# Optimization experiments

Measured on AMD Instinct MI355X. Metric: run time of the kernel, lower is better.

Reference implementation:

```python
import jax, jax.numpy as jnp
import numpy as np

B, F, T, L = 65536, 512, 8, 4


def setup_inputs() -> dict:
    key = jax.random.key(0)
    k1, k2, k3, k4, k5 = jax.random.split(key, 5)
    scale = 1.0 / np.sqrt(F)  # keep the 4-deep cross stack numerically tame
    return {
        "x": jax.random.normal(k1, (B, F), dtype=jnp.float32),
        "cross_w": jax.random.normal(k2, (L, F), dtype=jnp.float32) * scale,
        "cross_b": jax.random.normal(k3, (L, F), dtype=jnp.float32) * 0.1,
        "W_out": jax.random.normal(k4, (F, T), dtype=jnp.float32) * scale,
        "b_out": jax.random.normal(k5, (T,), dtype=jnp.float32) * 0.1,
    }


def reference(x, cross_w, cross_b, W_out, b_out):
    # DCN cross layers. torch does bmm(x0[:, :, None], x[:, None, :]) -> [B,F,F]
    # then tensordot with weights over the last axis; algebraically identical to
    # x0 * (x . w), which we compute directly (no O(B*F*F) intermediate).
    x0 = x
    for i in range(L):  # small fixed layer loop
        s = jnp.einsum("bf,f->b", x, cross_w[i])  # [B]
        x = x0 * s[:, None] + cross_b[i] + x
    return x @ W_out + b_out  # final Linear [B, T]
```

## Files before the change

kernel.cpp:

```cpp
#include <hip/hip_runtime.h>
#include <hip/hip_bf16.h>


typedef float v4f __attribute__((ext_vector_type(4)));
typedef float f32x4 __attribute__((ext_vector_type(4)));
typedef short s16x8 __attribute__((ext_vector_type(8)));

__device__ __forceinline__ short f2bf(float v) {
  return __builtin_bit_cast(short, __float2bfloat16(v));
}
__device__ __forceinline__ float bf2f(short s) {
  return __uint_as_float(((unsigned)(unsigned short)s) << 16);
}

template<int CTRL>
__device__ __forceinline__ float dpp_add(float v) {
  int t = __builtin_amdgcn_update_dpp(0, __float_as_int(v), CTRL, 0xF, 0xF, true);
  return v + __int_as_float(t);
}
__device__ __forceinline__ float wave_reduce(float v) {
  v = dpp_add<0x111>(v); v = dpp_add<0x112>(v); v = dpp_add<0x114>(v);
  v = dpp_add<0x118>(v); v = dpp_add<0x142>(v); v = dpp_add<0x143>(v);
  return v;
}

__global__ __launch_bounds__(256, 4) void cross_mfma(
    const float* __restrict__ x, const float* __restrict__ cw,
    const float* __restrict__ cb, const float* __restrict__ Wo,
    const float* __restrict__ bo, float* __restrict__ out)
{
  __shared__ s16x8 Bh[16][64];
  __shared__ s16x8 Bl[16][64];
  __shared__ float ct[4][16][17];
  __shared__ float egs[12];

  const int tid = threadIdx.x, lane = tid & 63, wv = tid >> 6;

  for (int slot = tid; slot < 1024; slot += 256) {
    const int s = slot >> 6, l = slot & 63;
    const int c = l & 15, k0 = s * 32 + ((l >> 4) << 3);
    float f[8];
    if (c < 4) {
      v4f a = *(const v4f*)(cw + c * 512 + k0);
      v4f b = *(const v4f*)(cw + c * 512 + k0 + 4);
      #pragma unroll
      for (int j = 0; j < 4; ++j) { f[j] = a[j]; f[4 + j] = b[j]; }
    } else if (c < 12) {
      #pragma unroll
      for (int j = 0; j < 8; ++j) f[j] = Wo[(k0 + j) * 8 + (c - 4)];
    } else {
      #pragma unroll
      for (int j = 0; j < 8; ++j) f[j] = 0.f;
    }
    s16x8 h, lo;
    #pragma unroll
    for (int j = 0; j < 8; ++j) {
      h[j]  = f2bf(f[j]);
      lo[j] = f2bf(f[j] - bf2f(h[j]));
    }
    Bh[s][l] = h;
    Bl[s][l] = lo;
  }

  if (wv == 0) {
    const int f0 = lane << 3;
    v4f d0a = *(const v4f*)(cb + f0),        d0b = *(const v4f*)(cb + f0 + 4);
    v4f c1a = *(const v4f*)(cb + 512 + f0),  c1b = *(const v4f*)(cb + 512 + f0 + 4);
    v4f c2a = *(const v4f*)(cb + 1024 + f0), c2b = *(const v4f*)(cb + 1024 + f0 + 4);
    v4f c3a = *(const v4f*)(cb + 1536 + f0), c3b = *(const v4f*)(cb + 1536 + f0 + 4);
    v4f w1a = *(const v4f*)(cw + 512 + f0),  w1b = *(const v4f*)(cw + 512 + f0 + 4);
    v4f w2a = *(const v4f*)(cw + 1024 + f0), w2b = *(const v4f*)(cw + 1024 + f0 + 4);
    v4f w3a = *(const v4f*)(cw + 1536 + f0), w3b = *(const v4f*)(cw + 1536 + f0 + 4);
    float e1p = 0.f, e2p = 0.f, e3p = 0.f;
    v4f dA = d0a, dB = d0b;
    #pragma unroll
    for (int e = 0; e < 4; ++e) e1p += dA[e] * w1a[e] + dB[e] * w1b[e];
    dA += c1a; dB += c1b;
    #pragma unroll
    for (int e = 0; e < 4; ++e) e2p += dA[e] * w2a[e] + dB[e] * w2b[e];
    dA += c2a; dB += c2b;
    #pragma unroll
    for (int e = 0; e < 4; ++e) e3p += dA[e] * w3a[e] + dB[e] * w3b[e];
    dA += c3a; dB += c3b;
    float gp[8] = {0.f,0.f,0.f,0.f,0.f,0.f,0.f,0.f};
    #pragma unroll
    for (int e = 0; e < 4; ++e) {
      const float* wra = Wo + (f0 + e) * 8;
      const float* wrb = Wo + (f0 + 4 + e) * 8;
      #pragma unroll
      for (int t = 0; t < 8; ++t) gp[t] += dA[e] * wra[t] + dB[e] * wrb[t];
    }
    e1p = wave_reduce(e1p); e2p = wave_reduce(e2p); e3p = wave_reduce(e3p);
    #pragma unroll
    for (int t = 0; t < 8; ++t) gp[t] = wave_reduce(gp[t]);
    if (lane == 63) {
      egs[0] = e1p; egs[1] = e2p; egs[2] = e3p;
      #pragma unroll
      for (int t = 0; t < 8; ++t) egs[3 + t] = gp[t] + bo[t];
    }
  }
  __syncthreads();

  const int row0 = (blockIdx.x << 6) + (wv << 4);
  const float* xr = x + (size_t)(row0 + (lane & 15)) * 512 + ((lane >> 4) << 3);
  const float e1 = egs[0], e2 = egs[1], e3 = egs[2];
  float gg[8];
  #pragma unroll
  for (int t = 0; t < 8; ++t) gg[t] = egs[3 + t];

  f32x4 acc = {0.f, 0.f, 0.f, 0.f};
  v4f pa = *(const v4f*)(xr), pb = *(const v4f*)(xr + 4);
  #pragma unroll
  for (int s = 0; s < 16; ++s) {
    v4f na = pa, nb = pb;
    if (s < 15) {
      na = *(const v4f*)(xr + (s + 1) * 32);
      nb = *(const v4f*)(xr + (s + 1) * 32 + 4);
    }
    const s16x8 bh = Bh[s][lane];
    const s16x8 bl = Bl[s][lane];
    s16x8 ah, al;
    #pragma unroll
    for (int j = 0; j < 4; ++j) {
      ah[j]     = f2bf(pa[j]); al[j]     = f2bf(pa[j] - bf2f(ah[j]));
      ah[4 + j] = f2bf(pb[j]); al[4 + j] = f2bf(pb[j] - bf2f(ah[4 + j]));
    }
    acc = __builtin_amdgcn_mfma_f32_16x16x32_bf16(ah, bh, acc, 0, 0, 0);
    acc = __builtin_amdgcn_mfma_f32_16x16x32_bf16(al, bh, acc, 0, 0, 0);
    acc = __builtin_amdgcn_mfma_f32_16x16x32_bf16(ah, bl, acc, 0, 0, 0);
    pa = na; pb = nb;
  }

  #pragma unroll
  for (int j = 0; j < 4; ++j)
    ct[wv][((lane >> 4) << 2) + j][lane & 15] = acc[j];
  if (lane < 16) {
    const float u0 = ct[wv][lane][0], u1 = ct[wv][lane][1];
    const float u2 = ct[wv][lane][2], u3 = ct[wv][lane][3];
    const float cc1 = 1.f + u0;
    const float cc2 = fmaf(cc1, u1, cc1) + e1;
    const float cc3 = fmaf(cc2, u2, cc2) + e2;
    const float cc4 = fmaf(cc3, u3, cc3) + e3;
    v4f o0, o1;
    #pragma unroll
    for (int t = 0; t < 4; ++t) {
      o0[t] = fmaf(cc4, ct[wv][lane][4 + t], gg[t]);
      o1[t] = fmaf(cc4, ct[wv][lane][8 + t], gg[4 + t]);
    }
    float* op = out + (size_t)(row0 + lane) * 8;
    *(v4f*)(op)     = o0;
    *(v4f*)(op + 4) = o1;
  }
}

extern "C" void kernel_launch(void* const* d_in, const int* in_sizes, int n_in,
                              void* d_out, int out_size, void* d_ws, size_t ws_size,
                              hipStream_t stream) {
  const float* x  = (const float*)d_in[0];
  const float* cw = (const float*)d_in[1];
  const float* cb = (const float*)d_in[2];
  const float* Wo = (const float*)d_in[3];
  const float* bo = (const float*)d_in[4];
  float* out = (float*)d_out;
  const int B = in_sizes[0] / 512;
  hipLaunchKernelGGL(cross_mfma, dim3(B >> 6), dim3(256), 0, stream,
                     x, cw, cb, Wo, bo, out);
}
```

Before: 30.63 us.

## Split weight-table prep into separate kernel and stream x with deeper prefetch

Moves the bf16 weight-table and bias-constant construction out of every block into a small pre-kernel that writes them to workspace. The main kernel then loads the table into registers, drops shared-memory staging and the block barrier, and prefetches x three steps ahead. It also removes the low-part correction on the weights, using two MFMAs per step instead of three. That lowers weight precision to bf16 plus a split of x only, and adds a second launch plus higher register pressure from 16 held fragments.

```diff
diff --git a/kernel.cpp b/kernel.cpp
--- a/kernel.cpp
+++ b/kernel.cpp
@@ -24,46 +24,35 @@
   return v;
 }
 
-__global__ __launch_bounds__(256, 4) void cross_mfma(
-    const float* __restrict__ x, const float* __restrict__ cw,
-    const float* __restrict__ cb, const float* __restrict__ Wo,
-    const float* __restrict__ bo, float* __restrict__ out)
+__global__ __launch_bounds__(64) void build_tab(
+    const float* __restrict__ cw, const float* __restrict__ cb,
+    const float* __restrict__ Wo, const float* __restrict__ bo, void* ws)
 {
-  __shared__ s16x8 Bh[16][64];
-  __shared__ s16x8 Bl[16][64];
-  __shared__ float ct[4][16][17];
-  __shared__ float egs[12];
+  s16x8* Bt = (s16x8*)ws;
+  float* egs = (float*)((char*)ws + 16384);
+  const int s = blockIdx.x, l = threadIdx.x;
+  const int c = l & 15, k0 = s * 32 + ((l >> 4) << 3);
 
-  const int tid = threadIdx.x, lane = tid & 63, wv = tid >> 6;
+  float f[8];
+  if (c < 4) {
+    v4f a = *(const v4f*)(cw + c * 512 + k0);
+    v4f b = *(const v4f*)(cw + c * 512 + k0 + 4);
+    #pragma unroll
+    for (int j = 0; j < 4; ++j) { f[j] = a[j]; f[4 + j] = b[j]; }
+  } else if (c < 12) {
+    #pragma unroll
+    for (int j = 0; j < 8; ++j) f[j] = Wo[(k0 + j) * 8 + (c - 4)];
+  } else {
+    #pragma unroll
+    for (int j = 0; j < 8; ++j) f[j] = 0.f;
+  }
+  s16x8 h;
+  #pragma unroll
+  for (int j = 0; j < 8; ++j) h[j] = f2bf(f[j]);
+  Bt[s * 64 + l] = h;
 
-  for (int slot = tid; slot < 1024; slot += 256) {
-    const int s = slot >> 6, l = slot & 63;
-    const int c = l & 15, k0 = s * 32 + ((l >> 4) << 3);
-    float f[8];
-    if (c < 4) {
-      v4f a = *(const v4f*)(cw + c * 512 + k0);
-      v4f b = *(const v4f*)(cw + c * 512 + k0 + 4);
-      #pragma unroll
-      for (int j = 0; j < 4; ++j) { f[j] = a[j]; f[4 + j] = b[j]; }
-    } else if (c < 12) {
-      #pragma unroll
-      for (int j = 0; j < 8; ++j) f[j] = Wo[(k0 + j) * 8 + (c - 4)];
-    } else {
-      #pragma unroll
-      for (int j = 0; j < 8; ++j) f[j] = 0.f;
-    }
-    s16x8 h, lo;
-    #pragma unroll
-    for (int j = 0; j < 8; ++j) {
-      h[j]  = f2bf(f[j]);
-      lo[j] = f2bf(f[j] - bf2f(h[j]));
-    }
-    Bh[s][l] = h;
-    Bl[s][l] = lo;
-  }
-
-  if (wv == 0) {
-    const int f0 = lane << 3;
+  if (s == 0) {
+    const int f0 = l << 3;
     v4f d0a = *(const v4f*)(cb + f0),        d0b = *(const v4f*)(cb + f0 + 4);
     v4f c1a = *(const v4f*)(cb + 512 + f0),  c1b = *(const v4f*)(cb + 512 + f0 + 4);
     v4f c2a = *(const v4f*)(cb + 1024 + f0), c2b = *(const v4f*)(cb + 1024 + f0 + 4);
@@ -93,47 +82,65 @@
     e1p = wave_reduce(e1p); e2p = wave_reduce(e2p); e3p = wave_reduce(e3p);
     #pragma unroll
     for (int t = 0; t < 8; ++t) gp[t] = wave_reduce(gp[t]);
-    if (lane == 63) {
+    if (l == 63) {
       egs[0] = e1p; egs[1] = e2p; egs[2] = e3p;
       #pragma unroll
       for (int t = 0; t < 8; ++t) egs[3 + t] = gp[t] + bo[t];
     }
   }
-  __syncthreads();
+}
 
-  const int row0 = (blockIdx.x << 6) + (wv << 4);
-  const float* xr = x + (size_t)(row0 + (lane & 15)) * 512 + ((lane >> 4) << 3);
+__global__ __launch_bounds__(256, 4) void cross_stream(
+    const float* __restrict__ x, const void* __restrict__ ws,
+    float* __restrict__ out)
+{
+  __shared__ float ct[4][16][17];
+
+  const int tid = threadIdx.x, lane = tid & 63, wv = tid >> 6;
+  const s16x8* Bt = (const s16x8*)ws;
+  const float* egs = (const float*)((const char*)ws + 16384);
+
+  s16x8 Bf[16];
+  #pragma unroll
+  for (int s = 0; s < 16; ++s) Bf[s] = Bt[s * 64 + lane];
+
   const float e1 = egs[0], e2 = egs[1], e3 = egs[2];
   float gg[8];
   #pragma unroll
   for (int t = 0; t < 8; ++t) gg[t] = egs[3 + t];
 
+  const int row0 = (blockIdx.x << 6) + (wv << 4);
+  const float* xr = x + (size_t)(row0 + (lane & 15)) * 512 + ((lane >> 4) << 3);
+
   f32x4 acc = {0.f, 0.f, 0.f, 0.f};
-  v4f pa = *(const v4f*)(xr), pb = *(const v4f*)(xr + 4);
+  v4f xa[3], xb[3];
+  #pragma unroll
+  for (int p = 0; p < 3; ++p) {
+    xa[p] = *(const v4f*)(xr + p * 32);
+    xb[p] = *(const v4f*)(xr + p * 32 + 4);
+  }
   #pragma unroll
   for (int s = 0; s < 16; ++s) {
-    v4f na = pa, nb = pb;
-    if (s < 15) {
-      na = *(const v4f*)(xr + (s + 1) * 32);
-      nb = *(const v4f*)(xr + (s + 1) * 32 + 4);
+    const int cur = s % 3;
+    const v4f pa = xa[cur], pb = xb[cur];
+    if (s + 3 < 16) {
+      xa[cur] = *(const v4f*)(xr + (s + 3) * 32);
+      xb[cur] = *(const v4f*)(xr + (s + 3) * 32 + 4);
     }
-    const s16x8 bh = Bh[s][lane];
-    const s16x8 bl = Bl[s][lane];
     s16x8 ah, al;
     #pragma unroll
     for (int j = 0; j < 4; ++j) {
       ah[j]     = f2bf(pa[j]); al[j]     = f2bf(pa[j] - bf2f(ah[j]));
       ah[4 + j] = f2bf(pb[j]); al[4 + j] = f2bf(pb[j] - bf2f(ah[4 + j]));
     }
-    acc = __builtin_amdgcn_mfma_f32_16x16x32_bf16(ah, bh, acc, 0, 0, 0);
-    acc = __builtin_amdgcn_mfma_f32_16x16x32_bf16(al, bh, acc, 0, 0, 0);
-    acc = __builtin_amdgcn_mfma_f32_16x16x32_bf16(ah, bl, acc, 0, 0, 0);
-    pa = na; pb = nb;
+    acc = __builtin_amdgcn_mfma_f32_16x16x32_bf16(ah, Bf[s], acc, 0, 0, 0);
+    acc = __builtin_amdgcn_mfma_f32_16x16x32_bf16(al, Bf[s], acc, 0, 0, 0);
   }
 
   #pragma unroll
   for (int j = 0; j < 4; ++j)
     ct[wv][((lane >> 4) << 2) + j][lane & 15] = acc[j];
+  __builtin_amdgcn_s_waitcnt(0);
   if (lane < 16) {
     const float u0 = ct[wv][lane][0], u1 = ct[wv][lane][1];
     const float u2 = ct[wv][lane][2], u3 = ct[wv][lane][3];
@@ -163,6 +170,8 @@
   const float* bo = (const float*)d_in[4];
   float* out = (float*)d_out;
   const int B = in_sizes[0] / 512;
-  hipLaunchKernelGGL(cross_mfma, dim3(B >> 6), dim3(256), 0, stream,
-                     x, cw, cb, Wo, bo, out);
+  hipLaunchKernelGGL(build_tab, dim3(16), dim3(64), 0, stream,
+                     cw, cb, Wo, bo, d_ws);
+  hipLaunchKernelGGL(cross_stream, dim3(B >> 6), dim3(256), 0, stream,
+                     x, d_ws, out);
 }
```

Result: slower. 31.37 us (+2.4%).

## Deepen x prefetch, drop low-bf16 weight split, compute constants per wave

Applied to the files above, without the earlier changes.

The x row chunks are now prefetched six steps ahead, with the first six loads issued before the shared-memory weight staging, so global latency overlaps setup. The low-order bf16 part of the weights is removed, which cuts one MFMA per step and halves the weight staging in LDS, at some cost in precision. Each wave now computes the bias-chain constants itself and broadcasts them with a shuffle, which removes the shared egs buffer and its dependence on wave 0. This adds redundant work across waves and raises register pressure from the 12 prefetch vectors.

```diff
diff --git a/kernel.cpp b/kernel.cpp
--- a/kernel.cpp
+++ b/kernel.cpp
@@ -24,20 +24,29 @@
   return v;
 }
 
-__global__ __launch_bounds__(256, 4) void cross_mfma(
+__global__ __launch_bounds__(256, 4) void cross_one(
     const float* __restrict__ x, const float* __restrict__ cw,
     const float* __restrict__ cb, const float* __restrict__ Wo,
     const float* __restrict__ bo, float* __restrict__ out)
 {
   __shared__ s16x8 Bh[16][64];
-  __shared__ s16x8 Bl[16][64];
   __shared__ float ct[4][16][17];
-  __shared__ float egs[12];
 
   const int tid = threadIdx.x, lane = tid & 63, wv = tid >> 6;
+  const int row0 = (blockIdx.x << 6) + (wv << 4);
+  const float* xr = x + (size_t)(row0 + (lane & 15)) * 512 + ((lane >> 4) << 3);
 
-  for (int slot = tid; slot < 1024; slot += 256) {
-    const int s = slot >> 6, l = slot & 63;
+  v4f xa[6], xb[6];
+  #pragma unroll
+  for (int p = 0; p < 6; ++p) {
+    xa[p] = *(const v4f*)(xr + p * 32);
+    xb[p] = *(const v4f*)(xr + p * 32 + 4);
+  }
+
+  #pragma unroll
+  for (int slot = 0; slot < 4; ++slot) {
+    const int s = (tid >> 6) + (slot << 2);
+    const int l = tid & 63;
     const int c = l & 15, k0 = s * 32 + ((l >> 4) << 3);
     float f[8];
     if (c < 4) {
@@ -52,17 +61,35 @@
       #pragma unroll
       for (int j = 0; j < 8; ++j) f[j] = 0.f;
     }
-    s16x8 h, lo;
+    s16x8 h;
     #pragma unroll
-    for (int j = 0; j < 8; ++j) {
-      h[j]  = f2bf(f[j]);
-      lo[j] = f2bf(f[j] - bf2f(h[j]));
+    for (int j = 0; j < 8; ++j) h[j] = f2bf(f[j]);
+    Bh[s][l] = h;
+  }
+  __syncthreads();
+
+  f32x4 acc = {0.f, 0.f, 0.f, 0.f};
+  #pragma unroll
+  for (int s = 0; s < 16; ++s) {
+    const int cur = s % 6;
+    const v4f pa = xa[cur], pb = xb[cur];
+    if (s + 6 < 16) {
+      xa[cur] = *(const v4f*)(xr + (s + 6) * 32);
+      xb[cur] = *(const v4f*)(xr + (s + 6) * 32 + 4);
     }
-    Bh[s][l] = h;
-    Bl[s][l] = lo;
+    const s16x8 bh = Bh[s][lane];
+    s16x8 ah, al;
+    #pragma unroll
+    for (int j = 0; j < 4; ++j) {
+      ah[j]     = f2bf(pa[j]); al[j]     = f2bf(pa[j] - bf2f(ah[j]));
+      ah[4 + j] = f2bf(pb[j]); al[4 + j] = f2bf(pb[j] - bf2f(ah[4 + j]));
+    }
+    acc = __builtin_amdgcn_mfma_f32_16x16x32_bf16(ah, bh, acc, 0, 0, 0);
+    acc = __builtin_amdgcn_mfma_f32_16x16x32_bf16(al, bh, acc, 0, 0, 0);
   }
 
-  if (wv == 0) {
+  float e1, e2, e3, gg[8];
+  {
     const int f0 = lane << 3;
     v4f d0a = *(const v4f*)(cb + f0),        d0b = *(const v4f*)(cb + f0 + 4);
     v4f c1a = *(const v4f*)(cb + 512 + f0),  c1b = *(const v4f*)(cb + 512 + f0 + 4);
@@ -93,47 +120,15 @@
     e1p = wave_reduce(e1p); e2p = wave_reduce(e2p); e3p = wave_reduce(e3p);
     #pragma unroll
     for (int t = 0; t < 8; ++t) gp[t] = wave_reduce(gp[t]);
-    if (lane == 63) {
-      egs[0] = e1p; egs[1] = e2p; egs[2] = e3p;
-      #pragma unroll
-      for (int t = 0; t < 8; ++t) egs[3 + t] = gp[t] + bo[t];
-    }
-  }
-  __syncthreads();
-
-  const int row0 = (blockIdx.x << 6) + (wv << 4);
-  const float* xr = x + (size_t)(row0 + (lane & 15)) * 512 + ((lane >> 4) << 3);
-  const float e1 = egs[0], e2 = egs[1], e3 = egs[2];
-  float gg[8];
-  #pragma unroll
-  for (int t = 0; t < 8; ++t) gg[t] = egs[3 + t];
-
-  f32x4 acc = {0.f, 0.f, 0.f, 0.f};
-  v4f pa = *(const v4f*)(xr), pb = *(const v4f*)(xr + 4);
-  #pragma unroll
-  for (int s = 0; s < 16; ++s) {
-    v4f na = pa, nb = pb;
-    if (s < 15) {
-      na = *(const v4f*)(xr + (s + 1) * 32);
-      nb = *(const v4f*)(xr + (s + 1) * 32 + 4);
-    }
-    const s16x8 bh = Bh[s][lane];
-    const s16x8 bl = Bl[s][lane];
-    s16x8 ah, al;
+    e1 = __shfl(e1p, 63); e2 = __shfl(e2p, 63); e3 = __shfl(e3p, 63);
     #pragma unroll
-    for (int j = 0; j < 4; ++j) {
-      ah[j]     = f2bf(pa[j]); al[j]     = f2bf(pa[j] - bf2f(ah[j]));
-      ah[4 + j] = f2bf(pb[j]); al[4 + j] = f2bf(pb[j] - bf2f(ah[4 + j]));
-    }
-    acc = __builtin_amdgcn_mfma_f32_16x16x32_bf16(ah, bh, acc, 0, 0, 0);
-    acc = __builtin_amdgcn_mfma_f32_16x16x32_bf16(al, bh, acc, 0, 0, 0);
-    acc = __builtin_amdgcn_mfma_f32_16x16x32_bf16(ah, bl, acc, 0, 0, 0);
-    pa = na; pb = nb;
+    for (int t = 0; t < 8; ++t) gg[t] = __shfl(gp[t], 63) + bo[t];
   }
 
   #pragma unroll
   for (int j = 0; j < 4; ++j)
     ct[wv][((lane >> 4) << 2) + j][lane & 15] = acc[j];
+  __builtin_amdgcn_s_waitcnt(0);
   if (lane < 16) {
     const float u0 = ct[wv][lane][0], u1 = ct[wv][lane][1];
     const float u2 = ct[wv][lane][2], u3 = ct[wv][lane][3];
@@ -163,6 +158,6 @@
   const float* bo = (const float*)d_in[4];
   float* out = (float*)d_out;
   const int B = in_sizes[0] / 512;
-  hipLaunchKernelGGL(cross_mfma, dim3(B >> 6), dim3(256), 0, stream,
+  hipLaunchKernelGGL(cross_one, dim3(B >> 6), dim3(256), 0, stream,
                      x, cw, cb, Wo, bo, out);
 }
```

Result: slower. 35.93 us (+17.3%).

## Stream x through LDS via global_load_lds double buffer; drop weight low-part MFMA

Applied to the files above, without the earlier changes.

Replaces the per-lane register prefetch of x with direct global-to-LDS async loads into a swizzled two-stage buffer per wave. The loads are issued before the weight-setup phase so they overlap with it. The kernel also drops the bf16 low-part split of the weight matrix, going from three MFMAs per k-step to two. This cuts LDS footprint and matrix work, but it lowers the precision of the weight operand and adds manual vmcnt/lgkmcnt waits that must stay correct.

```diff
diff --git a/kernel.cpp b/kernel.cpp
--- a/kernel.cpp
+++ b/kernel.cpp
@@ -24,17 +24,39 @@
   return v;
 }
 
-__global__ __launch_bounds__(256, 4) void cross_mfma(
+__global__ __launch_bounds__(256, 4) void cross_glds(
     const float* __restrict__ x, const float* __restrict__ cw,
     const float* __restrict__ cb, const float* __restrict__ Wo,
     const float* __restrict__ bo, float* __restrict__ out)
 {
   __shared__ s16x8 Bh[16][64];
-  __shared__ s16x8 Bl[16][64];
+  __shared__ float slab[2][4][512];
   __shared__ float ct[4][16][17];
   __shared__ float egs[12];
 
   const int tid = threadIdx.x, lane = tid & 63, wv = tid >> 6;
+  const int row0 = (blockIdx.x << 6) + (wv << 4);
+
+  const int prow = lane >> 3;
+  const int pchk = (lane & 7) ^ prow;
+  const float* srcA = x + (size_t)(row0 + prow) * 512 + (pchk << 2);
+  const float* srcB = srcA + 8 * 512;
+
+#define GLDS(srcp, dstp)                                                     \
+  __builtin_amdgcn_global_load_lds(                                          \
+      (const __attribute__((address_space(1))) float*)(srcp),                \
+      (__attribute__((address_space(3))) float*)(dstp), 16, 0, 0)
+#define STAGE(s, b) do {                                                     \
+    GLDS(srcA + (s) * 32, &slab[b][wv][0]);                                  \
+    GLDS(srcB + (s) * 32, &slab[b][wv][256]);                                \
+  } while (0)
+#define WAITV(n) do { asm volatile("s_waitcnt vmcnt(" #n ")" ::: "memory");  \
+                      __builtin_amdgcn_sched_barrier(0); } while (0)
+#define WAITL()  do { asm volatile("s_waitcnt lgkmcnt(0)" ::: "memory");     \
+                      __builtin_amdgcn_sched_barrier(0); } while (0)
+
+  STAGE(0, 0);
+  STAGE(1, 1);
 
   for (int slot = tid; slot < 1024; slot += 256) {
     const int s = slot >> 6, l = slot & 63;
@@ -52,14 +74,10 @@
       #pragma unroll
       for (int j = 0; j < 8; ++j) f[j] = 0.f;
     }
-    s16x8 h, lo;
+    s16x8 h;
     #pragma unroll
-    for (int j = 0; j < 8; ++j) {
-      h[j]  = f2bf(f[j]);
-      lo[j] = f2bf(f[j] - bf2f(h[j]));
-    }
+    for (int j = 0; j < 8; ++j) h[j] = f2bf(f[j]);
     Bh[s][l] = h;
-    Bl[s][l] = lo;
   }
 
   if (wv == 0) {
@@ -101,24 +119,23 @@
   }
   __syncthreads();
 
-  const int row0 = (blockIdx.x << 6) + (wv << 4);
-  const float* xr = x + (size_t)(row0 + (lane & 15)) * 512 + ((lane >> 4) << 3);
-  const float e1 = egs[0], e2 = egs[1], e3 = egs[2];
-  float gg[8];
-  #pragma unroll
-  for (int t = 0; t < 8; ++t) gg[t] = egs[3 + t];
+  const int rrow = lane & 15;
+  const int g    = (lane >> 4) << 1;
+  const int ro   = (rrow << 5) + ((g ^ (rrow & 7)) << 2);
+  const int ro1  = (rrow << 5) + (((g + 1) ^ (rrow & 7)) << 2);
+  const float* rp0 = &slab[0][wv][0];
+  const float* rp1 = &slab[1][wv][0];
 
   f32x4 acc = {0.f, 0.f, 0.f, 0.f};
-  v4f pa = *(const v4f*)(xr), pb = *(const v4f*)(xr + 4);
   #pragma unroll
   for (int s = 0; s < 16; ++s) {
-    v4f na = pa, nb = pb;
-    if (s < 15) {
-      na = *(const v4f*)(xr + (s + 1) * 32);
-      nb = *(const v4f*)(xr + (s + 1) * 32 + 4);
-    }
+    if (s < 15) { WAITV(2); } else { WAITV(0); }
+    const float* rp = (s & 1) ? rp1 : rp0;
+    const v4f pa = *(const v4f*)(rp + ro);
+    const v4f pb = *(const v4f*)(rp + ro1);
+    WAITL();
+    if (s + 2 < 16) STAGE(s + 2, s & 1);
     const s16x8 bh = Bh[s][lane];
-    const s16x8 bl = Bl[s][lane];
     s16x8 ah, al;
     #pragma unroll
     for (int j = 0; j < 4; ++j) {
@@ -127,13 +144,17 @@
     }
     acc = __builtin_amdgcn_mfma_f32_16x16x32_bf16(ah, bh, acc, 0, 0, 0);
     acc = __builtin_amdgcn_mfma_f32_16x16x32_bf16(al, bh, acc, 0, 0, 0);
-    acc = __builtin_amdgcn_mfma_f32_16x16x32_bf16(ah, bl, acc, 0, 0, 0);
-    pa = na; pb = nb;
   }
+
+  const float e1 = egs[0], e2 = egs[1], e3 = egs[2];
+  float gg[8];
+  #pragma unroll
+  for (int t = 0; t < 8; ++t) gg[t] = egs[3 + t];
 
   #pragma unroll
   for (int j = 0; j < 4; ++j)
     ct[wv][((lane >> 4) << 2) + j][lane & 15] = acc[j];
+  WAITL();
   if (lane < 16) {
     const float u0 = ct[wv][lane][0], u1 = ct[wv][lane][1];
     const float u2 = ct[wv][lane][2], u3 = ct[wv][lane][3];
@@ -151,6 +172,10 @@
     *(v4f*)(op)     = o0;
     *(v4f*)(op + 4) = o1;
   }
+#undef GLDS
+#undef STAGE
+#undef WAITV
+#undef WAITL
 }
 
 extern "C" void kernel_launch(void* const* d_in, const int* in_sizes, int n_in,
@@ -163,6 +188,6 @@
   const float* bo = (const float*)d_in[4];
   float* out = (float*)d_out;
   const int B = in_sizes[0] / 512;
-  hipLaunchKernelGGL(cross_mfma, dim3(B >> 6), dim3(256), 0, stream,
+  hipLaunchKernelGGL(cross_glds, dim3(B >> 6), dim3(256), 0, stream,
                      x, cw, cb, Wo, bo, out);
 }
```

Result: no change. 30.57 us (-0.2%).
